# Kernel tuning notes

Measured on AMD Instinct MI355X. Metric: run time of the kernel, lower is better.

Reference implementation:

```python
import jax, jax.numpy as jnp
import numpy as np

N, E, F_IN, OUT = 10000, 80000, 128, 32
H1, C1 = 8, 256   # conv1: heads=8, out_channels=256, concat=True
H2, C2 = 1, OUT   # conv2: heads=1, out_channels=OUT, concat=False
NEG_SLOPE = 0.2


def _add_self_loops(edge_index, edge_attr, n_nodes):
    # PyG fill_value='mean': self-loop edge_attr = mean of incoming edge attrs per dst node
    src, dst = edge_index[0], edge_index[1]
    s = jax.ops.segment_sum(edge_attr, dst, num_segments=n_nodes)
    cnt = jax.ops.segment_sum(jnp.ones((edge_attr.shape[0],), edge_attr.dtype), dst, num_segments=n_nodes)
    self_attr = s / jnp.maximum(cnt, 1.0)[:, None]
    loop = jnp.arange(n_nodes)
    return (jnp.concatenate([src, loop]), jnp.concatenate([dst, loop]),
            jnp.concatenate([edge_attr, self_attr], axis=0))


def _gatv2(x, src, dst, edge_attr, Wl, bl, Wr, br, We, att, bias, heads, out_ch, concat, n_nodes):
    xl = (x @ Wl + bl).reshape(n_nodes, heads, out_ch)   # source-side projection
    xr = (x @ Wr + br).reshape(n_nodes, heads, out_ch)   # target-side projection
    e = (edge_attr @ We).reshape(-1, heads, out_ch)      # edge feature projection (no bias in PyG)
    m = jax.nn.leaky_relu(xl[src] + xr[dst] + e, NEG_SLOPE)   # [Etot, H, C]
    logits = jnp.einsum('ehc,hc->eh', m, att)            # per-edge attention logits
    # segment softmax over edges grouped by destination node (stable)
    lmax = jax.ops.segment_max(logits, dst, num_segments=n_nodes)
    ex = jnp.exp(logits - lmax[dst])
    denom = jax.ops.segment_sum(ex, dst, num_segments=n_nodes)
    alpha = ex / denom[dst]                              # [Etot, H]
    out = jax.ops.segment_sum(xl[src] * alpha[:, :, None], dst, num_segments=n_nodes)  # [N, H, C]
    out = out.reshape(n_nodes, heads * out_ch) if concat else out.mean(axis=1)
    return out + bias


def setup_inputs() -> dict:
    key = jax.random.key(0)
    ks = jax.random.split(key, 17)
    s = 0.05
    return {
        'x': jax.random.normal(ks[0], (N, F_IN), jnp.float32),
        'edge_index': jax.random.randint(ks[1], (2, E), 0, N),
        'edge_attr': jax.random.normal(ks[2], (E, F_IN), jnp.float32),
        # conv1 params
        'Wl1': jax.random.normal(ks[3], (F_IN, H1 * C1), jnp.float32) * s,
        'bl1': jnp.zeros((H1 * C1,), jnp.float32),
        'Wr1': jax.random.normal(ks[4], (F_IN, H1 * C1), jnp.float32) * s,
        'br1': jnp.zeros((H1 * C1,), jnp.float32),
        'We1': jax.random.normal(ks[5], (F_IN, H1 * C1), jnp.float32) * s,
        'att1': jax.random.normal(ks[6], (H1, C1), jnp.float32) * s,
        'b1': jnp.zeros((H1 * C1,), jnp.float32),
        # conv2 params (input dim = H1*C1 = 2048)
        'Wl2': jax.random.normal(ks[7], (H1 * C1, H2 * C2), jnp.float32) * s,
        'bl2': jnp.zeros((H2 * C2,), jnp.float32),
        'Wr2': jax.random.normal(ks[8], (H1 * C1, H2 * C2), jnp.float32) * s,
        'br2': jnp.zeros((H2 * C2,), jnp.float32),
        'We2': jax.random.normal(ks[9], (F_IN, H2 * C2), jnp.float32) * s,
        'att2': jax.random.normal(ks[10], (H2, C2), jnp.float32) * s,
        'b2': jnp.zeros((C2,), jnp.float32),
    }


def reference(x, edge_index, edge_attr, Wl1, bl1, Wr1, br1, We1, att1, b1,
              Wl2, bl2, Wr2, br2, We2, att2, b2):
    # mode='eval': all dropouts are identity
    src, dst, ea = _add_self_loops(edge_index, edge_attr, N)
    h = _gatv2(x, src, dst, ea, Wl1, bl1, Wr1, br1, We1, att1, b1, H1, C1, True, N)
    h = jax.nn.relu(h)
    out = _gatv2(h, src, dst, ea, Wl2, bl2, Wr2, br2, We2, att2, b2, H2, C2, False, N)
    return jax.nn.relu(out)
```

## Files before the change

kernel.cpp:

```cpp
#include <hip/hip_runtime.h>
#include <hip/hip_bf16.h>

#define N_NODES 10000
#define N_EDGES 80000
#define ETOT (N_EDGES + N_NODES)
#define FD 128
#define D1 2048
#define D2 32
#define NEG 0.2f

typedef __hip_bfloat16 bf16;
typedef __attribute__((ext_vector_type(8))) short short8;
typedef __attribute__((ext_vector_type(4))) short short4v;
typedef __attribute__((ext_vector_type(4))) float f32x4;

__device__ __forceinline__ bf16 f2b(float v){ return __float2bfloat16(v); }
__device__ __forceinline__ short f2bs(float v){ bf16 t=__float2bfloat16(v); return *(short*)&t; }
__device__ __forceinline__ float b2fs(short s){
    return __uint_as_float(((unsigned int)(unsigned short)s) << 16);
}

__global__ void k_deg(const int* __restrict__ ei, int* __restrict__ deg){
    int e = blockIdx.x*256 + threadIdx.x;
    if(e < N_EDGES) atomicAdd(&deg[ei[N_EDGES+e]], 1);
}

__global__ void k_scan(const int* __restrict__ deg, int* __restrict__ row_start,
                       int* __restrict__ cursor){
    __shared__ int sdata[256];
    int tid = threadIdx.x;
    const int CH = 40;
    int base = tid*CH;
    int lsum = 0;
    for(int i=0;i<CH;i++){
        int v=base+i;
        if(v<N_NODES){ lsum += deg[v]+1; cursor[v]=0; }
    }
    sdata[tid]=lsum; __syncthreads();
    for(int off=1; off<256; off<<=1){
        int val = (tid>=off)? sdata[tid-off] : 0;
        __syncthreads();
        sdata[tid] += val;
        __syncthreads();
    }
    int run = (tid>0)? sdata[tid-1] : 0;
    for(int i=0;i<CH;i++){
        int v=base+i;
        if(v<=N_NODES){
            row_start[v]=run;
            if(v<N_NODES) run += deg[v]+1;
        }
    }
}

__global__ void k_fill(const int* __restrict__ ei, const int* __restrict__ row_start,
                       int* __restrict__ cursor, int* __restrict__ ecsr,
                       int* __restrict__ srcs, int* __restrict__ dsts){
    int e = blockIdx.x*256 + threadIdx.x;
    if(e >= ETOT) return;
    int src = (e < N_EDGES) ? ei[e]          : (e - N_EDGES);
    int dst = (e < N_EDGES) ? ei[N_EDGES+e]  : (e - N_EDGES);
    int p = atomicAdd(&cursor[dst], 1);
    int pos = row_start[dst]+p;
    ecsr[pos] = e;
    srcs[pos] = src;
    dsts[pos] = dst;
}

__global__ void k_selfmean(const int* __restrict__ ecsr, const int* __restrict__ row_start,
                           const float* __restrict__ ea, float* __restrict__ self_attr){
    int v = blockIdx.x, t = threadIdx.x;
    int start=row_start[v], end=row_start[v+1];
    float s=0.f; int cnt=0;
    for(int i=start;i<end;i++){
        int e=ecsr[i];
        if(e<N_EDGES){ s += ea[(size_t)e*FD+t]; cnt++; }
    }
    self_attr[(size_t)v*FD+t] = s / fmaxf((float)cnt, 1.f);
}

__global__ void k_packAll(const float* __restrict__ We1, const float* __restrict__ Wl1,
                          const float* __restrict__ Wr1, const float* __restrict__ Wl2,
                          const float* __restrict__ Wr2, const float* __restrict__ We2,
                          short* __restrict__ Wb1, short* __restrict__ Wbl1,
                          short* __restrict__ Wbr1, short* __restrict__ Wb2,
                          short* __restrict__ Wb2e){
    int y = blockIdx.y;
    int idx = blockIdx.x*256 + threadIdx.x;
    if(y < 3){
        const float* W = (y==0)? We1 : (y==1)? Wl1 : Wr1;
        short* Wb      = (y==0)? Wb1 : (y==1)? Wbl1 : Wbr1;
        int k = idx >> 11, c = idx & 2047;
        int cb = c>>4, col = c&15, kc = k>>5, quad = (k>>3)&3, j = k&7;
        Wb[((size_t)(cb*4+kc)*64 + quad*16 + col)*8 + j] = f2bs(W[idx]);
    } else {
        if(idx < 131072){
            int k = idx >> 6, c = idx & 63;
            float v = (c < 32) ? Wl2[k*32 + c] : Wr2[k*32 + (c-32)];
            int cb = c>>4, col = c&15, kc = k>>5, quad = (k>>3)&3, j = k&7;
            Wb2[((size_t)(cb*64+kc)*64 + quad*16 + col)*8 + j] = f2bs(v);
        } else if(idx < 131072+4096){
            int t = idx - 131072;
            int k = t >> 5, c = t & 31;
            int cb = c>>4, col = c&15, kc = k>>5, quad = (k>>3)&3, j = k&7;
            Wb2e[((size_t)(cb*4+kc)*64 + quad*16 + col)*8 + j] = f2bs(We2[t]);
        }
    }
}

__global__ __launch_bounds__(256) void k_gemm1m(const float* __restrict__ x,
        const short* __restrict__ Wbl, const float* __restrict__ bl, bf16* __restrict__ outl,
        const short* __restrict__ Wbr, const float* __restrict__ br, bf16* __restrict__ outr){
    const short* Wb   = (blockIdx.y==0)? Wbl : Wbr;
    const float* bias = (blockIdx.y==0)? bl  : br;
    bf16* outp        = (blockIdx.y==0)? outl: outr;
    __shared__ short a_lds[64*128];
    __shared__ float tile[4][32][20];
    int tid = threadIdx.x;
    int r0 = blockIdx.x*64;
    for(int q=tid; q<64*32; q+=256){
        int m=q>>5, kq=(q&31)*4;
        int gr=r0+m;
        float4 v4 = {0,0,0,0};
        if(gr<N_NODES) v4 = *(const float4*)(x+(size_t)gr*FD+kq);
        int kc=kq>>5, quad=(kq>>3)&3, j=kq&7;
        short4v sv; sv[0]=f2bs(v4.x); sv[1]=f2bs(v4.y); sv[2]=f2bs(v4.z); sv[3]=f2bs(v4.w);
        *(short4v*)&a_lds[((kc*4+quad)*64+m)*8+j] = sv;
    }
    __syncthreads();
    int w=tid>>6, lane=tid&63, quad=lane>>4, col=lane&15;
    int arow=lane&31, half=lane>>5;
    short8 af[4][4];
    #pragma unroll
    for(int mg=0;mg<4;mg++)
        #pragma unroll
        for(int kc=0;kc<4;kc++)
            af[mg][kc] = *(const short8*)&a_lds[((kc*4+quad)*64+mg*16+col)*8];
    int orowA = r0 + arow;
    int orowB = r0 + 32 + arow;
    for(int cbl=0;cbl<32;cbl++){
        int cbg = w*32+cbl;
        f32x4 c0={0,0,0,0}, c1={0,0,0,0}, c2={0,0,0,0}, c3={0,0,0,0};
        #pragma unroll
        for(int kc=0;kc<4;kc++){
            short8 bfr = *(const short8*)(Wb + ((size_t)(cbg*4+kc)*64 + lane)*8);
            c0 = __builtin_amdgcn_mfma_f32_16x16x32_bf16(af[0][kc], bfr, c0, 0,0,0);
            c1 = __builtin_amdgcn_mfma_f32_16x16x32_bf16(af[1][kc], bfr, c1, 0,0,0);
            c2 = __builtin_amdgcn_mfma_f32_16x16x32_bf16(af[2][kc], bfr, c2, 0,0,0);
            c3 = __builtin_amdgcn_mfma_f32_16x16x32_bf16(af[3][kc], bfr, c3, 0,0,0);
        }
        int cg = cbg*16 + half*8;
        float4 b0 = *(const float4*)(bias+cg);
        float4 b1v = *(const float4*)(bias+cg+4);
        float bb[8]={b0.x,b0.y,b0.z,b0.w,b1v.x,b1v.y,b1v.z,b1v.w};
        #pragma unroll
        for(int rg=0;rg<4;rg++){
            tile[w][quad*4+rg][col]    = c0[rg];
            tile[w][16+quad*4+rg][col] = c1[rg];
        }
        {
            float4 t0 = *(float4*)&tile[w][arow][half*8];
            float4 t1 = *(float4*)&tile[w][arow][half*8+4];
            if(orowA < N_NODES){
                float tv[8]={t0.x,t0.y,t0.z,t0.w,t1.x,t1.y,t1.z,t1.w};
                short8 ov;
                #pragma unroll
                for(int j=0;j<8;j++) ov[j] = f2bs(tv[j]+bb[j]);
                *(short8*)(outp + (size_t)orowA*D1 + cg) = ov;
            }
        }
        #pragma unroll
        for(int rg=0;rg<4;rg++){
            tile[w][quad*4+rg][col]    = c2[rg];
            tile[w][16+quad*4+rg][col] = c3[rg];
        }
        {
            float4 t0 = *(float4*)&tile[w][arow][half*8];
            float4 t1 = *(float4*)&tile[w][arow][half*8+4];
            if(orowB < N_NODES){
                float tv[8]={t0.x,t0.y,t0.z,t0.w,t1.x,t1.y,t1.z,t1.w};
                short8 ov;
                #pragma unroll
                for(int j=0;j<8;j++) ov[j] = f2bs(tv[j]+bb[j]);
                *(short8*)(outp + (size_t)orowB*D1 + cg) = ov;
            }
        }
    }
}

__global__ __launch_bounds__(256) void k_logit1(const int* __restrict__ ecsr,
        const int* __restrict__ srcs, const int* __restrict__ dsts,
        const float* __restrict__ ea, const float* __restrict__ self_attr,
        const bf16* __restrict__ xl1, const bf16* __restrict__ xr1,
        const short* __restrict__ Wb, const short* __restrict__ Wb2e,
        const float* __restrict__ att1,
        float* __restrict__ logits1p, float* __restrict__ e2){
    __shared__ short a_lds[64*128];
    __shared__ float tile[4][32][20];
    __shared__ int ssrc[64], sdst[64], sed[64];
    int tid = threadIdx.x;
    int i0 = blockIdx.x*64;
    if(tid<64){
        int i=i0+tid; if(i>=ETOT) i=ETOT-1;
        sed[tid]=ecsr[i]; ssrc[tid]=srcs[i]; sdst[tid]=dsts[i];
    }
    __syncthreads();
    for(int q=tid; q<64*32; q+=256){
        int m=q>>5, kq=(q&31)*4;
        int e=sed[m];
        const float* sp = (e<N_EDGES)? (ea+(size_t)e*FD+kq) : (self_attr+(size_t)(e-N_EDGES)*FD+kq);
        float4 v4 = *(const float4*)sp;
        int kc=kq>>5, quad=(kq>>3)&3, j=kq&7;
        short4v sv; sv[0]=f2bs(v4.x); sv[1]=f2bs(v4.y); sv[2]=f2bs(v4.z); sv[3]=f2bs(v4.w);
        *(short4v*)&a_lds[((kc*4+quad)*64+m)*8+j] = sv;
    }
    __syncthreads();
    int w=tid>>6, lane=tid&63, quad=lane>>4, col=lane&15;
    int arow=lane&31, half=lane>>5;
    short8 af[4][4];
    #pragma unroll
    for(int mg=0;mg<4;mg++)
        #pragma unroll
        for(int kc=0;kc<4;kc++)
            af[mg][kc] = *(const short8*)&a_lds[((kc*4+quad)*64+mg*16+col)*8];
    const bf16* xlpA = xl1 + (size_t)ssrc[arow]*D1;
    const bf16* xrpA = xr1 + (size_t)sdst[arow]*D1;
    const bf16* xlpB = xl1 + (size_t)ssrc[32+arow]*D1;
    const bf16* xrpB = xr1 + (size_t)sdst[32+arow]*D1;
    float acch[4]={0.f,0.f,0.f,0.f};
    for(int cbl=0;cbl<32;cbl++){
        int cbg = w*32+cbl;
        f32x4 c0={0,0,0,0}, c1={0,0,0,0}, c2={0,0,0,0}, c3={0,0,0,0};
        #pragma unroll
        for(int kc=0;kc<4;kc++){
            short8 bfr = *(const short8*)(Wb + ((size_t)(cbg*4+kc)*64 + lane)*8);
            c0 = __builtin_amdgcn_mfma_f32_16x16x32_bf16(af[0][kc], bfr, c0, 0,0,0);
            c1 = __builtin_amdgcn_mfma_f32_16x16x32_bf16(af[1][kc], bfr, c1, 0,0,0);
            c2 = __builtin_amdgcn_mfma_f32_16x16x32_bf16(af[2][kc], bfr, c2, 0,0,0);
            c3 = __builtin_amdgcn_mfma_f32_16x16x32_bf16(af[3][kc], bfr, c3, 0,0,0);
        }
        int hs = cbl>>4;
        int cg = cbg*16 + half*8;
        float4 a0 = *(const float4*)(att1+cg);
        float4 a1 = *(const float4*)(att1+cg+4);
        float av[8]={a0.x,a0.y,a0.z,a0.w,a1.x,a1.y,a1.z,a1.w};
        #pragma unroll
        for(int rg=0;rg<4;rg++){
            tile[w][quad*4+rg][col]    = c0[rg];
            tile[w][16+quad*4+rg][col] = c1[rg];
        }
        {
            float4 t0 = *(float4*)&tile[w][arow][half*8];
            float4 t1 = *(float4*)&tile[w][arow][half*8+4];
            short8 xlv = *(const short8*)(xlpA + cg);
            short8 xrv = *(const short8*)(xrpA + cg);
            float tv[8]={t0.x,t0.y,t0.z,t0.w,t1.x,t1.y,t1.z,t1.w};
            float acc = acch[hs];
            #pragma unroll
            for(int j=0;j<8;j++){
                float m = tv[j] + b2fs(xlv[j]) + b2fs(xrv[j]);
                m = (m>0.f)? m : NEG*m;
                acc += av[j]*m;
            }
            acch[hs] = acc;
        }
        #pragma unroll
        for(int rg=0;rg<4;rg++){
            tile[w][quad*4+rg][col]    = c2[rg];
            tile[w][16+quad*4+rg][col] = c3[rg];
        }
        {
            float4 t0 = *(float4*)&tile[w][arow][half*8];
            float4 t1 = *(float4*)&tile[w][arow][half*8+4];
            short8 xlv = *(const short8*)(xlpB + cg);
            short8 xrv = *(const short8*)(xrpB + cg);
            float tv[8]={t0.x,t0.y,t0.z,t0.w,t1.x,t1.y,t1.z,t1.w};
            float acc = acch[2+hs];
            #pragma unroll
            for(int j=0;j<8;j++){
                float m = tv[j] + b2fs(xlv[j]) + b2fs(xrv[j]);
                m = (m>0.f)? m : NEG*m;
                acc += av[j]*m;
            }
            acch[2+hs] = acc;
        }
    }
    if(w<2){
        f32x4 c0={0,0,0,0}, c1={0,0,0,0}, c2={0,0,0,0}, c3={0,0,0,0};
        #pragma unroll
        for(int kc=0;kc<4;kc++){
            short8 bfr = *(const short8*)(Wb2e + ((size_t)(w*4+kc)*64 + lane)*8);
            c0 = __builtin_amdgcn_mfma_f32_16x16x32_bf16(af[0][kc], bfr, c0, 0,0,0);
            c1 = __builtin_amdgcn_mfma_f32_16x16x32_bf16(af[1][kc], bfr, c1, 0,0,0);
            c2 = __builtin_amdgcn_mfma_f32_16x16x32_bf16(af[2][kc], bfr, c2, 0,0,0);
            c3 = __builtin_amdgcn_mfma_f32_16x16x32_bf16(af[3][kc], bfr, c3, 0,0,0);
        }
        #pragma unroll
        for(int rg=0;rg<4;rg++){
            tile[w][quad*4+rg][col]    = c0[rg];
            tile[w][16+quad*4+rg][col] = c1[rg];
        }
        {
            int i=i0+arow;
            float4 t0 = *(float4*)&tile[w][arow][half*8];
            float4 t1 = *(float4*)&tile[w][arow][half*8+4];
            if(i<ETOT){
                *(float4*)(e2 + (size_t)i*32 + w*16 + half*8)     = t0;
                *(float4*)(e2 + (size_t)i*32 + w*16 + half*8 + 4) = t1;
            }
        }
        #pragma unroll
        for(int rg=0;rg<4;rg++){
            tile[w][quad*4+rg][col]    = c2[rg];
            tile[w][16+quad*4+rg][col] = c3[rg];
        }
        {
            int i=i0+32+arow;
            float4 t0 = *(float4*)&tile[w][arow][half*8];
            float4 t1 = *(float4*)&tile[w][arow][half*8+4];
            if(i<ETOT){
                *(float4*)(e2 + (size_t)i*32 + w*16 + half*8)     = t0;
                *(float4*)(e2 + (size_t)i*32 + w*16 + half*8 + 4) = t1;
            }
        }
    }
    #pragma unroll
    for(int r=0;r<4;r++) acch[r] += __shfl_xor(acch[r],32);
    if(lane<32){
        int iA=i0+arow;
        if(iA<ETOT){
            logits1p[(size_t)iA*8 + w*2  ] = acch[0];
            logits1p[(size_t)iA*8 + w*2+1] = acch[1];
        }
        int iB=i0+32+arow;
        if(iB<ETOT){
            logits1p[(size_t)iB*8 + w*2  ] = acch[2];
            logits1p[(size_t)iB*8 + w*2+1] = acch[3];
        }
    }
}

__global__ void k_agg1(const int* __restrict__ srcs, const int* __restrict__ row_start,
                       const float* __restrict__ logits1p, const bf16* __restrict__ xl1,
                       const float* __restrict__ b1, bf16* __restrict__ hb){
    int tid=threadIdx.x, v=blockIdx.x;
    int start=row_start[v], end=row_start[v+1];
    int w=tid>>6, lane=tid&63;
    int hpar = lane>>5;
    int myc = w*512 + lane*8;
    float ds0=0.f, ds1=0.f;
    for(int i=start+lane;i<end;i+=64){
        float2 lg = *(const float2*)(logits1p + (size_t)i*8 + w*2);
        ds0 += __expf(lg.x);
        ds1 += __expf(lg.y);
    }
    #pragma unroll
    for(int off=32;off>=1;off>>=1){
        ds0 += __shfl_xor(ds0,off);
        ds1 += __shfl_xor(ds1,off);
    }
    float rden = 1.f/((hpar==0)? ds0 : ds1);
    float acc[8]={0,0,0,0,0,0,0,0};
    for(int i=start;i<end;i++){
        int src = srcs[i];
        float2 lg = *(const float2*)(logits1p + (size_t)i*8 + w*2);
        float al = __expf((hpar==0)? lg.x : lg.y) * rden;
        short8 xv = *(const short8*)(xl1 + (size_t)src*D1 + myc);
        #pragma unroll
        for(int j=0;j<8;j++) acc[j] += al*b2fs(xv[j]);
    }
    float4 bb0=*(const float4*)(b1+myc), bb1=*(const float4*)(b1+myc+4);
    float bv[8]={bb0.x,bb0.y,bb0.z,bb0.w,bb1.x,bb1.y,bb1.z,bb1.w};
    short8 ov;
    #pragma unroll
    for(int j=0;j<8;j++) ov[j] = f2bs(fmaxf(acc[j]+bv[j],0.f));
    *(short8*)(hb + (size_t)v*D1 + myc) = ov;
}

__global__ __launch_bounds__(256) void k_gemm2(const bf16* __restrict__ hb,
        const short* __restrict__ Wb2, const float* __restrict__ bl2,
        const float* __restrict__ br2, float* __restrict__ xl2, float* __restrict__ xr2){
    __shared__ float cacc[4][16][64];
    int tid=threadIdx.x, w=tid>>6, lane=tid&63, quad=lane>>4, col=lane&15;
    int r0 = blockIdx.x*16;
    const bf16* hp = hb + (size_t)(r0+col)*D1 + quad*8;
    f32x4 acc[4] = {{0,0,0,0},{0,0,0,0},{0,0,0,0},{0,0,0,0}};
    for(int kc=w*16; kc<w*16+16; kc++){
        short8 af = *(const short8*)(hp + kc*32);
        #pragma unroll
        for(int cb=0;cb<4;cb++){
            short8 bfr = *(const short8*)(Wb2 + ((size_t)(cb*64+kc)*64 + lane)*8);
            acc[cb] = __builtin_amdgcn_mfma_f32_16x16x32_bf16(af, bfr, acc[cb], 0,0,0);
        }
    }
    #pragma unroll
    for(int cb=0;cb<4;cb++)
        #pragma unroll
        for(int rg=0;rg<4;rg++)
            cacc[w][quad*4+rg][cb*16+col] = acc[cb][rg];
    __syncthreads();
    #pragma unroll
    for(int i=0;i<4;i++){
        int idx = tid + 256*i;
        int r = idx>>6, c = idx&63;
        float s = cacc[0][r][c]+cacc[1][r][c]+cacc[2][r][c]+cacc[3][r][c];
        int rr = r0 + r;
        if(c<32) xl2[rr*32+c]      = s + bl2[c];
        else     xr2[rr*32+(c-32)] = s + br2[c-32];
    }
}

__global__ void k_agg2f(const int* __restrict__ srcs, const int* __restrict__ row_start,
                        const float* __restrict__ e2, const float* __restrict__ xl2,
                        const float* __restrict__ xr2, const float* __restrict__ att2,
                        const float* __restrict__ b2v, float* __restrict__ out){
    int tid=threadIdx.x, v=blockIdx.x;
    int start=row_start[v], end=row_start[v+1];
    int le=tid>>5, c=tid&31;
    float xr2v = xr2[v*32+c];
    float attc = att2[c];
    float ds=0.f, acc=0.f;
    for(int i=start+le;i<end;i+=2){
        int src=srcs[i];
        float xlv = xl2[src*32+c];
        float m = e2[(size_t)i*32+c] + xlv + xr2v;
        m = fmaxf(m, NEG*m);
        float p = attc*m;
        #pragma unroll
        for(int off=16;off>=1;off>>=1) p += __shfl_down(p,off,32);
        p = __shfl(p, 0, 32);
        float ep = __expf(p);
        ds  += ep;
        acc += ep*xlv;
    }
    ds  += __shfl_xor(ds,32);
    acc += __shfl_xor(acc,32);
    if(tid<32) out[(size_t)v*D2+c] = fmaxf(acc/ds + b2v[c], 0.f);
}

extern "C" void kernel_launch(void* const* d_in, const int* in_sizes, int n_in,
                              void* d_out, int out_size, void* d_ws, size_t ws_size,
                              hipStream_t stream) {
    const float* x    = (const float*)d_in[0];
    const int*   ei   = (const int*)d_in[1];
    const float* ea   = (const float*)d_in[2];
    const float* Wl1  = (const float*)d_in[3];
    const float* bl1  = (const float*)d_in[4];
    const float* Wr1  = (const float*)d_in[5];
    const float* br1  = (const float*)d_in[6];
    const float* We1  = (const float*)d_in[7];
    const float* att1 = (const float*)d_in[8];
    const float* b1   = (const float*)d_in[9];
    const float* Wl2  = (const float*)d_in[10];
    const float* bl2  = (const float*)d_in[11];
    const float* Wr2  = (const float*)d_in[12];
    const float* br2  = (const float*)d_in[13];
    const float* We2  = (const float*)d_in[14];
    const float* att2 = (const float*)d_in[15];
    const float* b2v  = (const float*)d_in[16];
    float* out = (float*)d_out;

    char* ws = (char*)d_ws;
    size_t off = 0;
    auto alloc = [&](size_t bytes)->char* {
        char* p = ws + off;
        off += (bytes + 255) & ~(size_t)255;
        return p;
    };
    float* self_attr = (float*)alloc((size_t)N_NODES*FD*4);
    int*   deg       = (int*)  alloc((size_t)N_NODES*4);
    int*   cursor    = (int*)  alloc((size_t)N_NODES*4);
    int*   row_start = (int*)  alloc((size_t)(N_NODES+1)*4);
    int*   ecsr      = (int*)  alloc((size_t)ETOT*4);
    int*   srcs      = (int*)  alloc((size_t)ETOT*4);
    int*   dsts      = (int*)  alloc((size_t)ETOT*4);
    float* logits1p  = (float*)alloc((size_t)ETOT*8*4);
    float* e2        = (float*)alloc((size_t)ETOT*32*4);
    bf16*  xl1       = (bf16*) alloc((size_t)N_NODES*D1*2);
    bf16*  xr1       = (bf16*) alloc((size_t)N_NODES*D1*2);
    bf16*  hb        = (bf16*) alloc((size_t)N_NODES*D1*2);
    float* xl2       = (float*)alloc((size_t)N_NODES*D2*4);
    float* xr2       = (float*)alloc((size_t)N_NODES*D2*4);
    short* Wb1       = (short*)alloc((size_t)FD*D1*2);
    short* Wbl1      = (short*)alloc((size_t)FD*D1*2);
    short* Wbr1      = (short*)alloc((size_t)FD*D1*2);
    short* Wb2       = (short*)alloc((size_t)D1*64*2);
    short* Wb2e      = (short*)alloc((size_t)FD*D2*2);
    (void)ws_size; (void)in_sizes; (void)n_in; (void)out_size;

    hipMemsetAsync(deg, 0, (size_t)N_NODES*4, stream);

    k_deg<<<(N_EDGES+255)/256, 256, 0, stream>>>(ei, deg);
    k_scan<<<1, 256, 0, stream>>>(deg, row_start, cursor);
    k_fill<<<(ETOT+255)/256, 256, 0, stream>>>(ei, row_start, cursor, ecsr, srcs, dsts);
    k_selfmean<<<N_NODES, 128, 0, stream>>>(ecsr, row_start, ea, self_attr);
    dim3 gp(1024, 4);
    k_packAll<<<gp, 256, 0, stream>>>(We1, Wl1, Wr1, Wl2, Wr2, We2,
                                      Wb1, Wbl1, Wbr1, Wb2, Wb2e);

    dim3 g1((N_NODES+63)/64, 2);
    k_gemm1m<<<g1, 256, 0, stream>>>(x, Wbl1, bl1, xl1, Wbr1, br1, xr1);

    k_logit1<<<(ETOT+63)/64, 256, 0, stream>>>(ecsr, srcs, dsts, ea, self_attr,
                                               xl1, xr1, Wb1, Wb2e, att1, logits1p, e2);
    k_agg1<<<N_NODES, 256, 0, stream>>>(srcs, row_start, logits1p, xl1, b1, hb);

    k_gemm2<<<N_NODES/16, 256, 0, stream>>>(hb, Wb2, bl2, br2, xl2, xr2);
    k_agg2f<<<N_NODES, 64, 0, stream>>>(srcs, row_start, e2, xl2, xr2, att2, b2v, out);
}
```

Before: 422.8 us.

## Vectorize selfmean, pack logit math into float2, unroll agg1, batch agg2 nodes per block

```diff
diff --git a/kernel.cpp b/kernel.cpp
--- a/kernel.cpp
+++ b/kernel.cpp
@@ -13,6 +13,7 @@
 typedef __attribute__((ext_vector_type(8))) short short8;
 typedef __attribute__((ext_vector_type(4))) short short4v;
 typedef __attribute__((ext_vector_type(4))) float f32x4;
+typedef __attribute__((ext_vector_type(2))) float f32x2;
 
 __device__ __forceinline__ bf16 f2b(float v){ return __float2bfloat16(v); }
 __device__ __forceinline__ short f2bs(float v){ bf16 t=__float2bfloat16(v); return *(short*)&t; }
@@ -69,14 +70,25 @@
 
 __global__ void k_selfmean(const int* __restrict__ ecsr, const int* __restrict__ row_start,
                            const float* __restrict__ ea, float* __restrict__ self_attr){
-    int v = blockIdx.x, t = threadIdx.x;
+    __shared__ float ssum[4][FD];
+    __shared__ int scnt[4];
+    int v = blockIdx.x, tid = threadIdx.x;
+    int eg = tid>>5, lane = tid&31;
     int start=row_start[v], end=row_start[v+1];
-    float s=0.f; int cnt=0;
-    for(int i=start;i<end;i++){
+    float4 s={0,0,0,0}; int cnt=0;
+    for(int i=start+eg;i<end;i+=4){
         int e=ecsr[i];
-        if(e<N_EDGES){ s += ea[(size_t)e*FD+t]; cnt++; }
-    }
-    self_attr[(size_t)v*FD+t] = s / fmaxf((float)cnt, 1.f);
+        if(e<N_EDGES){
+            float4 vv = *(const float4*)(ea+(size_t)e*FD+lane*4);
+            s.x+=vv.x; s.y+=vv.y; s.z+=vv.z; s.w+=vv.w; cnt++;
+        }
+    }
+    *(float4*)&ssum[eg][lane*4] = s;
+    if(lane==0) scnt[eg]=cnt;
+    __syncthreads();
+    float tot = ssum[0][tid]+ssum[1][tid]+ssum[2][tid]+ssum[3][tid];
+    int c = scnt[0]+scnt[1]+scnt[2]+scnt[3];
+    self_attr[(size_t)v*FD+tid] = tot / fmaxf((float)c, 1.f);
 }
 
 __global__ void k_packAll(const float* __restrict__ We1, const float* __restrict__ Wl1,
@@ -227,7 +239,7 @@
     const bf16* xrpA = xr1 + (size_t)sdst[arow]*D1;
     const bf16* xlpB = xl1 + (size_t)ssrc[32+arow]*D1;
     const bf16* xrpB = xr1 + (size_t)sdst[32+arow]*D1;
-    float acch[4]={0.f,0.f,0.f,0.f};
+    f32x2 accv[4] = {{0,0},{0,0},{0,0},{0,0}};
     for(int cbl=0;cbl<32;cbl++){
         int cbg = w*32+cbl;
         f32x4 c0={0,0,0,0}, c1={0,0,0,0}, c2={0,0,0,0}, c3={0,0,0,0};
@@ -243,7 +255,7 @@
         int cg = cbg*16 + half*8;
         float4 a0 = *(const float4*)(att1+cg);
         float4 a1 = *(const float4*)(att1+cg+4);
-        float av[8]={a0.x,a0.y,a0.z,a0.w,a1.x,a1.y,a1.z,a1.w};
+        f32x2 avp[4] = {{a0.x,a0.y},{a0.z,a0.w},{a1.x,a1.y},{a1.z,a1.w}};
         #pragma unroll
         for(int rg=0;rg<4;rg++){
             tile[w][quad*4+rg][col]    = c0[rg];
@@ -254,15 +266,17 @@
             float4 t1 = *(float4*)&tile[w][arow][half*8+4];
             short8 xlv = *(const short8*)(xlpA + cg);
             short8 xrv = *(const short8*)(xrpA + cg);
-            float tv[8]={t0.x,t0.y,t0.z,t0.w,t1.x,t1.y,t1.z,t1.w};
-            float acc = acch[hs];
+            f32x2 tvp[4]={{t0.x,t0.y},{t0.z,t0.w},{t1.x,t1.y},{t1.z,t1.w}};
+            f32x2 acc = accv[hs];
             #pragma unroll
-            for(int j=0;j<8;j++){
-                float m = tv[j] + b2fs(xlv[j]) + b2fs(xrv[j]);
-                m = (m>0.f)? m : NEG*m;
-                acc += av[j]*m;
+            for(int p=0;p<4;p++){
+                f32x2 xlf = {b2fs(xlv[2*p]), b2fs(xlv[2*p+1])};
+                f32x2 xrf = {b2fs(xrv[2*p]), b2fs(xrv[2*p+1])};
+                f32x2 m = tvp[p] + xlf + xrf;
+                m = __builtin_elementwise_max(m, m*NEG);
+                acc += avp[p]*m;
             }
-            acch[hs] = acc;
+            accv[hs] = acc;
         }
         #pragma unroll
         for(int rg=0;rg<4;rg++){
@@ -274,15 +288,17 @@
             float4 t1 = *(float4*)&tile[w][arow][half*8+4];
             short8 xlv = *(const short8*)(xlpB + cg);
             short8 xrv = *(const short8*)(xrpB + cg);
-            float tv[8]={t0.x,t0.y,t0.z,t0.w,t1.x,t1.y,t1.z,t1.w};
-            float acc = acch[2+hs];
+            f32x2 tvp[4]={{t0.x,t0.y},{t0.z,t0.w},{t1.x,t1.y},{t1.z,t1.w}};
+            f32x2 acc = accv[2+hs];
             #pragma unroll
-            for(int j=0;j<8;j++){
-                float m = tv[j] + b2fs(xlv[j]) + b2fs(xrv[j]);
-                m = (m>0.f)? m : NEG*m;
-                acc += av[j]*m;
+            for(int p=0;p<4;p++){
+                f32x2 xlf = {b2fs(xlv[2*p]), b2fs(xlv[2*p+1])};
+                f32x2 xrf = {b2fs(xrv[2*p]), b2fs(xrv[2*p+1])};
+                f32x2 m = tvp[p] + xlf + xrf;
+                m = __builtin_elementwise_max(m, m*NEG);
+                acc += avp[p]*m;
             }
-            acch[2+hs] = acc;
+            accv[2+hs] = acc;
         }
     }
     if(w<2){
@@ -324,8 +340,12 @@
             }
         }
     }
-    #pragma unroll
-    for(int r=0;r<4;r++) acch[r] += __shfl_xor(acch[r],32);
+    float acch[4];
+    #pragma unroll
+    for(int r=0;r<4;r++){
+        acch[r] = accv[r].x + accv[r].y;
+        acch[r] += __shfl_xor(acch[r],32);
+    }
     if(lane<32){
         int iA=i0+arow;
         if(iA<ETOT){
@@ -361,13 +381,25 @@
     }
     float rden = 1.f/((hpar==0)? ds0 : ds1);
     float acc[8]={0,0,0,0,0,0,0,0};
-    for(int i=start;i<end;i++){
-        int src = srcs[i];
-        float2 lg = *(const float2*)(logits1p + (size_t)i*8 + w*2);
-        float al = __expf((hpar==0)? lg.x : lg.y) * rden;
-        short8 xv = *(const short8*)(xl1 + (size_t)src*D1 + myc);
-        #pragma unroll
-        for(int j=0;j<8;j++) acc[j] += al*b2fs(xv[j]);
+    int i=start;
+    for(; i+2<=end; i+=2){
+        int s0 = srcs[i], s1 = srcs[i+1];
+        float2 g0 = *(const float2*)(logits1p + (size_t)i*8 + w*2);
+        float2 g1 = *(const float2*)(logits1p + (size_t)(i+1)*8 + w*2);
+        float a0v = __expf((hpar==0)? g0.x : g0.y) * rden;
+        float a1v = __expf((hpar==0)? g1.x : g1.y) * rden;
+        short8 x0 = *(const short8*)(xl1 + (size_t)s0*D1 + myc);
+        short8 x1 = *(const short8*)(xl1 + (size_t)s1*D1 + myc);
+        #pragma unroll
+        for(int j=0;j<8;j++) acc[j] += a0v*b2fs(x0[j]) + a1v*b2fs(x1[j]);
+    }
+    if(i<end){
+        int s0 = srcs[i];
+        float2 g0 = *(const float2*)(logits1p + (size_t)i*8 + w*2);
+        float a0v = __expf((hpar==0)? g0.x : g0.y) * rden;
+        short8 x0 = *(const short8*)(xl1 + (size_t)s0*D1 + myc);
+        #pragma unroll
+        for(int j=0;j<8;j++) acc[j] += a0v*b2fs(x0[j]);
     }
     float4 bb0=*(const float4*)(b1+myc), bb1=*(const float4*)(b1+myc+4);
     float bv[8]={bb0.x,bb0.y,bb0.z,bb0.w,bb1.x,bb1.y,bb1.z,bb1.w};
@@ -414,9 +446,11 @@
                         const float* __restrict__ e2, const float* __restrict__ xl2,
                         const float* __restrict__ xr2, const float* __restrict__ att2,
                         const float* __restrict__ b2v, float* __restrict__ out){
-    int tid=threadIdx.x, v=blockIdx.x;
+    int tid=threadIdx.x;
+    int w=tid>>6, lane=tid&63;
+    int v=blockIdx.x*4+w;
     int start=row_start[v], end=row_start[v+1];
-    int le=tid>>5, c=tid&31;
+    int le=lane>>5, c=lane&31;
     float xr2v = xr2[v*32+c];
     float attc = att2[c];
     float ds=0.f, acc=0.f;
@@ -435,7 +469,7 @@
     }
     ds  += __shfl_xor(ds,32);
     acc += __shfl_xor(acc,32);
-    if(tid<32) out[(size_t)v*D2+c] = fmaxf(acc/ds + b2v[c], 0.f);
+    if(lane<32) out[(size_t)v*D2+c] = fmaxf(acc/ds + b2v[c], 0.f);
 }
 
 extern "C" void kernel_launch(void* const* d_in, const int* in_sizes, int n_in,
@@ -506,5 +540,5 @@
     k_agg1<<<N_NODES, 256, 0, stream>>>(srcs, row_start, logits1p, xl1, b1, hb);
 
     k_gemm2<<<N_NODES/16, 256, 0, stream>>>(hb, Wb2, bl2, br2, xl2, xr2);
-    k_agg2f<<<N_NODES, 64, 0, stream>>>(srcs, row_start, e2, xl2, xr2, att2, b2v, out);
-}
+    k_agg2f<<<N_NODES/4, 256, 0, stream>>>(srcs, row_start, e2, xl2, xr2, att2, b2v, out);
+}
```

Measured after the change: 428.6 us. Within noise of the previous version (+1.4%).
